# Performance work log

Hardware: AMD Instinct MI355X
Metric: run time of the kernel (lower is better)

## Reference

```python
import jax, jax.numpy as jnp
from jax import lax
import numpy as np

IN, H1, H2 = 16, 64, 1


def _init_lstm(key, in_dim, hid):
    k = 1.0 / np.sqrt(hid)
    k1, k2, k3, k4 = jax.random.split(key, 4)
    u = lambda kk, shp: jax.random.uniform(kk, shp, jnp.float32, -k, k)
    return u(k1, (4 * hid, in_dim)), u(k2, (4 * hid, hid)), u(k3, (4 * hid,)), u(k4, (4 * hid,))


def setup_inputs() -> dict:
    key = jax.random.key(0)
    kx, k1, k2, kf = jax.random.split(key, 4)
    x = jax.random.normal(kx, (4096, 256, IN), jnp.float32)
    w_ih1, w_hh1, b_ih1, b_hh1 = _init_lstm(k1, IN, H1)
    w_ih2, w_hh2, b_ih2, b_hh2 = _init_lstm(k2, H1, H2)
    kfw, kfb = jax.random.split(kf)
    fc_w = jax.random.uniform(kfw, (1, 1), jnp.float32, -1.0, 1.0)
    fc_b = jax.random.uniform(kfb, (1,), jnp.float32, -1.0, 1.0)
    return {"x": x,
            "w_ih1": w_ih1, "w_hh1": w_hh1, "b_ih1": b_ih1, "b_hh1": b_hh1,
            "w_ih2": w_ih2, "w_hh2": w_hh2, "b_ih2": b_ih2, "b_hh2": b_hh2,
            "fc_w": fc_w, "fc_b": fc_b}


def _lstm(x, w_ih, w_hh, b_ih, b_hh):
    # x: [B, T, in]; PyTorch gate order: i, f, g, o
    B = x.shape[0]
    H = w_hh.shape[1]
    # precompute input projection for all timesteps (big GEMM outside recurrence)
    xg = jnp.einsum('bti,gi->btg', x, w_ih) + b_ih + b_hh  # [B, T, 4H]

    def step(carry, xg_t):
        h, c = carry
        gates = xg_t + h @ w_hh.T  # [B, 4H]
        i, f, g, o = jnp.split(gates, 4, axis=-1)
        i = jax.nn.sigmoid(i)
        f = jax.nn.sigmoid(f)
        g = jnp.tanh(g)
        o = jax.nn.sigmoid(o)
        c = f * c + i * g
        h = o * jnp.tanh(c)
        return (h, c), h

    h0 = jnp.zeros((B, H), x.dtype)
    (_, _), hs = lax.scan(step, (h0, h0), jnp.swapaxes(xg, 0, 1))  # hs: [T, B, H]
    return jnp.swapaxes(hs, 0, 1)  # [B, T, H]


def reference(x, w_ih1, w_hh1, b_ih1, b_hh1, w_ih2, w_hh2, b_ih2, b_hh2, fc_w, fc_b):
    h = _lstm(x, w_ih1, w_hh1, b_ih1, b_hh1)   # [B, T, 64]
    h = _lstm(h, w_ih2, w_hh2, b_ih2, b_hh2)   # [B, T, 1]
    return h @ fc_w.T + fc_b                     # [B, T, 1]
```

## Files before the change

kernel.cpp:

```cpp
#include <hip/hip_runtime.h>

typedef float  f32x4  __attribute__((ext_vector_type(4)));
typedef __bf16 bf16x8 __attribute__((ext_vector_type(8)));
typedef unsigned short u16x8 __attribute__((ext_vector_type(8)));

#define NL2E (-1.44269504088896f)
#define TL2E ( 2.88539008177793f)

__device__ __forceinline__ float sigm_z(float z) {
    return __builtin_amdgcn_rcpf(1.0f + __builtin_amdgcn_exp2f(z));
}
__device__ __forceinline__ float tanh_z(float z) {
    return 1.0f - 2.0f * __builtin_amdgcn_rcpf(1.0f + __builtin_amdgcn_exp2f(z));
}

__global__ __launch_bounds__(256, 1) void lstm_fused(
    const float* __restrict__ x,
    const float* __restrict__ w_ih1,
    const float* __restrict__ w_hh1,
    const float* __restrict__ b_ih1, const float* __restrict__ b_hh1,
    const float* __restrict__ w_ih2,
    const float* __restrict__ w_hh2,
    const float* __restrict__ b_ih2, const float* __restrict__ b_hh2,
    const float* __restrict__ fc_w, const float* __restrict__ fc_b,
    float* __restrict__ out)
{
    __shared__ unsigned short A_h[2 * 16 * 64];
    __shared__ unsigned short Xc[2 * 16 * 16 * 32];
    __shared__ float Pre2[2][64];

    const int tid = threadIdx.x;
    const int wv  = tid >> 6;
    const int l   = tid & 63;
    const int q   = l & 15;
    const int hi  = l >> 4;
    const int b0  = blockIdx.x << 4;
    const int he  = (wv << 4) + q;
    const int sw  = (q & 7) << 4;

    ((u16x8*)A_h)[tid] = (u16x8){0,0,0,0,0,0,0,0};

    bf16x8 Bf[4][3];
    #pragma unroll
    for (int g = 0; g < 4; ++g) {
        const float sc = (g == 2) ? TL2E : NL2E;
        const int n = (g << 6) + (wv << 4) + q;
        #pragma unroll
        for (int ks = 0; ks < 3; ++ks) {
            bf16x8 tmp;
            #pragma unroll
            for (int j = 0; j < 8; ++j) {
                const int k = ks * 32 + hi * 8 + j;
                float v = 0.f;
                if (k < 64)      v = w_hh1[n * 64 + k];
                else if (k < 80) v = w_ih1[n * 16 + (k - 64)];
                tmp[j] = (__bf16)(sc * v);
            }
            Bf[g][ks] = tmp;
        }
    }
    bf16x8 B2[2];
    {
        const float sc2 = (q == 2) ? TL2E : NL2E;
        #pragma unroll
        for (int ks = 0; ks < 2; ++ks) {
            bf16x8 tmp;
            #pragma unroll
            for (int j = 0; j < 8; ++j) {
                const int k = ks * 32 + hi * 8 + j;
                const float v = (q < 4) ? w_ih2[q * 64 + k] : 0.f;
                tmp[j] = (__bf16)(sc2 * v);
            }
            B2[ks] = tmp;
        }
    }

    float accb[4];
    #pragma unroll
    for (int g = 0; g < 4; ++g) {
        const float sc = (g == 2) ? TL2E : NL2E;
        accb[g] = sc * (b_ih1[(g << 6) + he] + b_hh1[(g << 6) + he]);
    }

    const float w2si = NL2E * w_hh2[0], w2sf = NL2E * w_hh2[1];
    const float w2sg = TL2E * w_hh2[2], w2so = NL2E * w_hh2[3];
    const float nb2i = NL2E * (b_ih2[0] + b_hh2[0]);
    const float nb2f = NL2E * (b_ih2[1] + b_hh2[1]);
    const float tb2g = TL2E * (b_ih2[2] + b_hh2[2]);
    const float nb2o = NL2E * (b_ih2[3] + b_hh2[3]);
    const float fcw = fc_w[0], fcb = fc_b[0];

    const int bx = tid >> 4, part = tid & 15;
    const int swx = (bx & 7) << 4;
    const unsigned xo0 = (unsigned)(bx * 1024 + (((part << 6) +  0) ^ swx));
    const unsigned xo1 = (unsigned)(bx * 1024 + (((part << 6) + 16) ^ swx));
    const unsigned xo2 = (unsigned)(bx * 1024 + (((part << 6) + 32) ^ swx));
    const unsigned xo3 = (unsigned)(bx * 1024 + (((part << 6) + 48) ^ swx));
    const float* xrow = x + (size_t)(b0 + bx) * 4096 + part * 16;

    f32x4 xq0, xq1, xq2, xq3;
    auto stage_x = [&](int bufoff) {
        bf16x8 lo, hw;
        #pragma unroll
        for (int j = 0; j < 4; ++j) {
            lo[j] = (__bf16)xq0[j]; lo[4 + j] = (__bf16)xq1[j];
            hw[j] = (__bf16)xq2[j]; hw[4 + j] = (__bf16)xq3[j];
        }
        const u16x8 z = {0,0,0,0,0,0,0,0};
        char* base = (char*)Xc + bufoff;
        *(u16x8*)(base + xo0) = __builtin_bit_cast(u16x8, lo);
        *(u16x8*)(base + xo1) = __builtin_bit_cast(u16x8, hw);
        *(u16x8*)(base + xo2) = z;
        *(u16x8*)(base + xo3) = z;
    };

    xq0 = ((const f32x4*)xrow)[0]; xq1 = ((const f32x4*)xrow)[1];
    xq2 = ((const f32x4*)xrow)[2]; xq3 = ((const f32x4*)xrow)[3];
    stage_x(0);
    {
        const float* p = xrow + 256;
        xq0 = ((const f32x4*)p)[0]; xq1 = ((const f32x4*)p)[1];
        xq2 = ((const f32x4*)p)[2]; xq3 = ((const f32x4*)p)[3];
    }

    const unsigned ar0 = (unsigned)((q * 128 +      hi * 16) ^ sw);
    const unsigned ar1 = (unsigned)((q * 128 + 64 + hi * 16) ^ sw);
    unsigned awb[4];
    #pragma unroll
    for (int j = 0; j < 4; ++j) {
        const int b = (hi << 2) + j;
        awb[j] = (unsigned)(b * 128 + ((he * 2) ^ ((b & 7) << 4)));
    }

    f32x4 c1 = {0.f, 0.f, 0.f, 0.f};
    float h2 = 0.f, c2 = 0.f;

    __syncthreads();

    #pragma unroll 2
    for (int t = 0; t < 256; ++t) {
        const int tt = t & 15;
        if (tt == 0 && t + 16 < 256) {
            stage_x(((((t >> 4) + 1) & 1)) << 14);
            if (t + 32 < 256) {
                const float* p = xrow + (t + 32) * 16;
                xq0 = ((const f32x4*)p)[0]; xq1 = ((const f32x4*)p)[1];
                xq2 = ((const f32x4*)p)[2]; xq3 = ((const f32x4*)p)[3];
            }
        }

        const int rb = ((t + 1) & 1) << 11;
        const u16x8 ra0 = *(const u16x8*)((const char*)A_h + rb + ar0);
        const u16x8 ra1 = *(const u16x8*)((const char*)A_h + rb + ar1);
        const u16x8 ra2 = *(const u16x8*)((const char*)Xc + (((t >> 4) & 1) << 14)
                                          + ((q * 1024 + (tt << 6) + (hi << 4)) ^ sw));

        if (wv == 1 && t >= 2 && l < 16) {
            const f32x4 p2 = *(const f32x4*)&Pre2[(t + 1) & 1][l << 2];
            const float zi = p2[0] + __builtin_fmaf(w2si, h2, nb2i);
            const float zf = p2[1] + __builtin_fmaf(w2sf, h2, nb2f);
            const float zg = p2[2] + __builtin_fmaf(w2sg, h2, tb2g);
            const float zo = p2[3] + __builtin_fmaf(w2so, h2, nb2o);
            const float i2 = sigm_z(zi), f2v = sigm_z(zf);
            const float g2v = tanh_z(zg), o2 = sigm_z(zo);
            c2 = __builtin_fmaf(f2v, c2, i2 * g2v);
            h2 = o2 * tanh_z(c2 * TL2E);
            out[(size_t)(b0 + l) * 256 + (t - 2)] = __builtin_fmaf(fcw, h2, fcb);
        }

        const bf16x8 a0 = __builtin_bit_cast(bf16x8, ra0);
        const bf16x8 a1 = __builtin_bit_cast(bf16x8, ra1);
        const bf16x8 a2 = __builtin_bit_cast(bf16x8, ra2);

        f32x4 g0 = {accb[0], accb[0], accb[0], accb[0]};
        f32x4 g1 = {accb[1], accb[1], accb[1], accb[1]};
        f32x4 g2 = {accb[2], accb[2], accb[2], accb[2]};
        f32x4 g3 = {accb[3], accb[3], accb[3], accb[3]};
        g0 = __builtin_amdgcn_mfma_f32_16x16x32_bf16(a0, Bf[0][0], g0, 0, 0, 0);
        g1 = __builtin_amdgcn_mfma_f32_16x16x32_bf16(a0, Bf[1][0], g1, 0, 0, 0);
        g2 = __builtin_amdgcn_mfma_f32_16x16x32_bf16(a0, Bf[2][0], g2, 0, 0, 0);
        g3 = __builtin_amdgcn_mfma_f32_16x16x32_bf16(a0, Bf[3][0], g3, 0, 0, 0);
        g0 = __builtin_amdgcn_mfma_f32_16x16x32_bf16(a1, Bf[0][1], g0, 0, 0, 0);
        g1 = __builtin_amdgcn_mfma_f32_16x16x32_bf16(a1, Bf[1][1], g1, 0, 0, 0);
        g2 = __builtin_amdgcn_mfma_f32_16x16x32_bf16(a1, Bf[2][1], g2, 0, 0, 0);
        g3 = __builtin_amdgcn_mfma_f32_16x16x32_bf16(a1, Bf[3][1], g3, 0, 0, 0);
        g0 = __builtin_amdgcn_mfma_f32_16x16x32_bf16(a2, Bf[0][2], g0, 0, 0, 0);
        g1 = __builtin_amdgcn_mfma_f32_16x16x32_bf16(a2, Bf[1][2], g1, 0, 0, 0);
        g2 = __builtin_amdgcn_mfma_f32_16x16x32_bf16(a2, Bf[2][2], g2, 0, 0, 0);
        g3 = __builtin_amdgcn_mfma_f32_16x16x32_bf16(a2, Bf[3][2], g3, 0, 0, 0);

        if (wv == 3) {
            f32x4 p4 = {0.f, 0.f, 0.f, 0.f};
            p4 = __builtin_amdgcn_mfma_f32_16x16x32_bf16(a0, B2[0], p4, 0, 0, 0);
            p4 = __builtin_amdgcn_mfma_f32_16x16x32_bf16(a1, B2[1], p4, 0, 0, 0);
            if (q < 4) {
                #pragma unroll
                for (int r = 0; r < 4; ++r) Pre2[t & 1][((hi << 2) + r) * 4 + q] = p4[r];
            }
        }

        unsigned short* AW = (unsigned short*)((char*)A_h + ((t & 1) << 11));
        #pragma unroll
        for (int j = 0; j < 4; ++j) {
            const float iv = sigm_z(g0[j]);
            const float fv = sigm_z(g1[j]);
            const float gv = tanh_z(g2[j]);
            const float ov = sigm_z(g3[j]);
            const float cn = __builtin_fmaf(fv, c1[j], iv * gv);
            c1[j] = cn;
            const float hv = ov * tanh_z(cn * TL2E);
            *(unsigned short*)((char*)AW + awb[j]) = __builtin_bit_cast(unsigned short, (__bf16)hv);
        }
        __syncthreads();
    }

    if (wv == 3) {
        const u16x8 ra0 = *(const u16x8*)((const char*)A_h + 2048 + ar0);
        const u16x8 ra1 = *(const u16x8*)((const char*)A_h + 2048 + ar1);
        f32x4 p4 = {0.f, 0.f, 0.f, 0.f};
        p4 = __builtin_amdgcn_mfma_f32_16x16x32_bf16(__builtin_bit_cast(bf16x8, ra0), B2[0], p4, 0, 0, 0);
        p4 = __builtin_amdgcn_mfma_f32_16x16x32_bf16(__builtin_bit_cast(bf16x8, ra1), B2[1], p4, 0, 0, 0);
        if (q < 4) {
            #pragma unroll
            for (int r = 0; r < 4; ++r) Pre2[0][((hi << 2) + r) * 4 + q] = p4[r];
        }
    }
    if (wv == 1 && l < 16) {
        const f32x4 p2 = *(const f32x4*)&Pre2[1][l << 2];
        const float zi = p2[0] + __builtin_fmaf(w2si, h2, nb2i);
        const float zf = p2[1] + __builtin_fmaf(w2sf, h2, nb2f);
        const float zg = p2[2] + __builtin_fmaf(w2sg, h2, tb2g);
        const float zo = p2[3] + __builtin_fmaf(w2so, h2, nb2o);
        const float i2 = sigm_z(zi), f2v = sigm_z(zf);
        const float g2v = tanh_z(zg), o2 = sigm_z(zo);
        c2 = __builtin_fmaf(f2v, c2, i2 * g2v);
        h2 = o2 * tanh_z(c2 * TL2E);
        out[(size_t)(b0 + l) * 256 + 254] = __builtin_fmaf(fcw, h2, fcb);
    }
    __syncthreads();
    if (wv == 1 && l < 16) {
        const f32x4 p2 = *(const f32x4*)&Pre2[0][l << 2];
        const float zi = p2[0] + __builtin_fmaf(w2si, h2, nb2i);
        const float zf = p2[1] + __builtin_fmaf(w2sf, h2, nb2f);
        const float zg = p2[2] + __builtin_fmaf(w2sg, h2, tb2g);
        const float zo = p2[3] + __builtin_fmaf(w2so, h2, nb2o);
        const float i2 = sigm_z(zi), f2v = sigm_z(zf);
        const float g2v = tanh_z(zg), o2 = sigm_z(zo);
        c2 = __builtin_fmaf(f2v, c2, i2 * g2v);
        h2 = o2 * tanh_z(c2 * TL2E);
        out[(size_t)(b0 + l) * 256 + 255] = __builtin_fmaf(fcw, h2, fcb);
    }
}

extern "C" void kernel_launch(void* const* d_in, const int* in_sizes, int n_in,
                              void* d_out, int out_size, void* d_ws, size_t ws_size,
                              hipStream_t stream) {
    (void)in_sizes; (void)n_in; (void)out_size; (void)d_ws; (void)ws_size;
    const float* x     = (const float*)d_in[0];
    const float* w_ih1 = (const float*)d_in[1];
    const float* w_hh1 = (const float*)d_in[2];
    const float* b_ih1 = (const float*)d_in[3];
    const float* b_hh1 = (const float*)d_in[4];
    const float* w_ih2 = (const float*)d_in[5];
    const float* w_hh2 = (const float*)d_in[6];
    const float* b_ih2 = (const float*)d_in[7];
    const float* b_hh2 = (const float*)d_in[8];
    const float* fc_w  = (const float*)d_in[9];
    const float* fc_b  = (const float*)d_in[10];
    lstm_fused<<<dim3(256), dim3(256), 0, stream>>>(
        x, w_ih1, w_hh1, b_ih1, b_hh1, w_ih2, w_hh2, b_ih2, b_hh2, fc_w, fc_b,
        (float*)d_out);
}
```

Baseline: 157.0 us.

## Halve batch rows per block to 8 and launch 512 blocks at two per CU

Each block now handles 8 batch rows instead of 16 and the grid doubles to 512 blocks, with launch bounds raised to two blocks per CU so the serial 256-step recurrence is spread across more CUs. Because the 16-row MFMA tile now holds only 8 real rows, each lane evaluates the LSTM cell for two rows rather than four, which shortens the per-step activation chain. Output for layer 2 is gathered into a small shared buffer and written as 16-wide vector stores instead of one scalar store per step, and odd block groups sleep briefly at start to stagger them. The cost is half of every MFMA doing wasted work on padding rows and more register pressure at two blocks per CU.

```diff
diff --git a/kernel.cpp b/kernel.cpp
--- a/kernel.cpp
+++ b/kernel.cpp
@@ -14,7 +14,7 @@
     return 1.0f - 2.0f * __builtin_amdgcn_rcpf(1.0f + __builtin_amdgcn_exp2f(z));
 }
 
-__global__ __launch_bounds__(256, 1) void lstm_fused(
+__global__ __launch_bounds__(256, 2) void lstm_fused(
     const float* __restrict__ x,
     const float* __restrict__ w_ih1,
     const float* __restrict__ w_hh1,
@@ -25,20 +25,31 @@
     const float* __restrict__ fc_w, const float* __restrict__ fc_b,
     float* __restrict__ out)
 {
-    __shared__ unsigned short A_h[2 * 16 * 64];
-    __shared__ unsigned short Xc[2 * 16 * 16 * 32];
-    __shared__ float Pre2[2][64];
+    __shared__ unsigned short A_h[2 * 8 * 64];
+    __shared__ unsigned short Xc[2 * 8 * 16 * 32];
+    __shared__ float Pre2[2][32];
+    __shared__ float Ybuf[8][16];
 
     const int tid = threadIdx.x;
     const int wv  = tid >> 6;
     const int l   = tid & 63;
     const int q   = l & 15;
     const int hi  = l >> 4;
-    const int b0  = blockIdx.x << 4;
+    const int b0  = blockIdx.x << 3;
     const int he  = (wv << 4) + q;
-    const int sw  = (q & 7) << 4;
-
-    ((u16x8*)A_h)[tid] = (u16x8){0,0,0,0,0,0,0,0};
+
+    if ((blockIdx.x >> 8) & 1) __builtin_amdgcn_s_sleep(7);
+
+    if (tid < 128) ((u16x8*)A_h)[tid] = (u16x8){0,0,0,0,0,0,0,0};
+    {
+        const int sb = tid >> 5, sr = tid & 31, st = sr >> 1, sh = sr & 1;
+        const u16x8 z = {0,0,0,0,0,0,0,0};
+        #pragma unroll
+        for (int buf = 0; buf < 2; ++buf) {
+            *(u16x8*)((char*)Xc + buf * 8192 + sb * 1024
+                      + ((st * 64 + 32 + sh * 16) ^ (sb << 4))) = z;
+        }
+    }
 
     bf16x8 Bf[4][3];
     #pragma unroll
@@ -90,49 +101,34 @@
     const float nb2o = NL2E * (b_ih2[3] + b_hh2[3]);
     const float fcw = fc_w[0], fcb = fc_b[0];
 
-    const int bx = tid >> 4, part = tid & 15;
-    const int swx = (bx & 7) << 4;
-    const unsigned xo0 = (unsigned)(bx * 1024 + (((part << 6) +  0) ^ swx));
-    const unsigned xo1 = (unsigned)(bx * 1024 + (((part << 6) + 16) ^ swx));
-    const unsigned xo2 = (unsigned)(bx * 1024 + (((part << 6) + 32) ^ swx));
-    const unsigned xo3 = (unsigned)(bx * 1024 + (((part << 6) + 48) ^ swx));
-    const float* xrow = x + (size_t)(b0 + bx) * 4096 + part * 16;
-
-    f32x4 xq0, xq1, xq2, xq3;
+    const int sb = tid >> 5, sr = tid & 31, st = sr >> 1, sh = sr & 1;
+    const unsigned xoff = (unsigned)(sb * 1024 + ((st * 64 + sh * 16) ^ (sb << 4)));
+    const float* xrow = x + (size_t)(b0 + sb) * 4096 + st * 16 + sh * 8;
+
+    f32x4 xqa, xqb;
+    auto ldx = [&](int t) {
+        const float* p = xrow + t * 16;
+        xqa = ((const f32x4*)p)[0]; xqb = ((const f32x4*)p)[1];
+    };
     auto stage_x = [&](int bufoff) {
-        bf16x8 lo, hw;
-        #pragma unroll
-        for (int j = 0; j < 4; ++j) {
-            lo[j] = (__bf16)xq0[j]; lo[4 + j] = (__bf16)xq1[j];
-            hw[j] = (__bf16)xq2[j]; hw[4 + j] = (__bf16)xq3[j];
-        }
-        const u16x8 z = {0,0,0,0,0,0,0,0};
-        char* base = (char*)Xc + bufoff;
-        *(u16x8*)(base + xo0) = __builtin_bit_cast(u16x8, lo);
-        *(u16x8*)(base + xo1) = __builtin_bit_cast(u16x8, hw);
-        *(u16x8*)(base + xo2) = z;
-        *(u16x8*)(base + xo3) = z;
+        bf16x8 v;
+        #pragma unroll
+        for (int j = 0; j < 4; ++j) { v[j] = (__bf16)xqa[j]; v[4 + j] = (__bf16)xqb[j]; }
+        *(u16x8*)((char*)Xc + bufoff + xoff) = __builtin_bit_cast(u16x8, v);
     };
-
-    xq0 = ((const f32x4*)xrow)[0]; xq1 = ((const f32x4*)xrow)[1];
-    xq2 = ((const f32x4*)xrow)[2]; xq3 = ((const f32x4*)xrow)[3];
-    stage_x(0);
-    {
-        const float* p = xrow + 256;
-        xq0 = ((const f32x4*)p)[0]; xq1 = ((const f32x4*)p)[1];
-        xq2 = ((const f32x4*)p)[2]; xq3 = ((const f32x4*)p)[3];
-    }
-
-    const unsigned ar0 = (unsigned)((q * 128 +      hi * 16) ^ sw);
-    const unsigned ar1 = (unsigned)((q * 128 + 64 + hi * 16) ^ sw);
-    unsigned awb[4];
-    #pragma unroll
-    for (int j = 0; j < 4; ++j) {
-        const int b = (hi << 2) + j;
-        awb[j] = (unsigned)(b * 128 + ((he * 2) ^ ((b & 7) << 4)));
-    }
-
-    f32x4 c1 = {0.f, 0.f, 0.f, 0.f};
+    ldx(0); stage_x(0); ldx(16);
+
+    const int rb = q & 7;
+    const unsigned ar0 = (unsigned)(rb * 128 + ((hi * 16)      ^ (rb << 4)));
+    const unsigned ar1 = (unsigned)(rb * 128 + ((64 + hi * 16) ^ (rb << 4)));
+    const unsigned xro = (unsigned)(rb * 1024);
+    const unsigned xrs = (unsigned)(hi * 16);
+    const int bA = ((hi & 1) << 2) + ((hi >> 1) << 1);
+    const int bB = bA + 1;
+    const unsigned awA = (unsigned)(bA * 128 + ((he * 2) ^ (bA << 4)));
+    const unsigned awB = (unsigned)(bB * 128 + ((he * 2) ^ (bB << 4)));
+
+    float cA = 0.f, cB = 0.f;
     float h2 = 0.f, c2 = 0.f;
 
     __syncthreads();
@@ -141,21 +137,17 @@
     for (int t = 0; t < 256; ++t) {
         const int tt = t & 15;
         if (tt == 0 && t + 16 < 256) {
-            stage_x(((((t >> 4) + 1) & 1)) << 14);
-            if (t + 32 < 256) {
-                const float* p = xrow + (t + 32) * 16;
-                xq0 = ((const f32x4*)p)[0]; xq1 = ((const f32x4*)p)[1];
-                xq2 = ((const f32x4*)p)[2]; xq3 = ((const f32x4*)p)[3];
-            }
-        }
-
-        const int rb = ((t + 1) & 1) << 11;
-        const u16x8 ra0 = *(const u16x8*)((const char*)A_h + rb + ar0);
-        const u16x8 ra1 = *(const u16x8*)((const char*)A_h + rb + ar1);
-        const u16x8 ra2 = *(const u16x8*)((const char*)Xc + (((t >> 4) & 1) << 14)
-                                          + ((q * 1024 + (tt << 6) + (hi << 4)) ^ sw));
-
-        if (wv == 1 && t >= 2 && l < 16) {
+            stage_x((((t >> 4) + 1) & 1) << 13);
+            if (t + 32 < 256) ldx(t + 32);
+        }
+
+        const int rbo = ((t + 1) & 1) << 10;
+        const u16x8 ra0 = *(const u16x8*)((const char*)A_h + rbo + ar0);
+        const u16x8 ra1 = *(const u16x8*)((const char*)A_h + rbo + ar1);
+        const u16x8 ra2 = *(const u16x8*)((const char*)Xc + (((t >> 4) & 1) << 13)
+                                          + xro + (((tt << 6) + xrs) ^ (rb << 4)));
+
+        if (wv == 1 && l < 8 && t >= 2) {
             const f32x4 p2 = *(const f32x4*)&Pre2[(t + 1) & 1][l << 2];
             const float zi = p2[0] + __builtin_fmaf(w2si, h2, nb2i);
             const float zf = p2[1] + __builtin_fmaf(w2sf, h2, nb2f);
@@ -165,7 +157,14 @@
             const float g2v = tanh_z(zg), o2 = sigm_z(zo);
             c2 = __builtin_fmaf(f2v, c2, i2 * g2v);
             h2 = o2 * tanh_z(c2 * TL2E);
-            out[(size_t)(b0 + l) * 256 + (t - 2)] = __builtin_fmaf(fcw, h2, fcb);
+            const int s = t - 2;
+            Ybuf[l][s & 15] = __builtin_fmaf(fcw, h2, fcb);
+            if ((s & 15) == 15) {
+                float* op = out + (size_t)(b0 + l) * 256 + (s - 15);
+                const f32x4* yb = (const f32x4*)Ybuf[l];
+                ((f32x4*)op)[0] = yb[0]; ((f32x4*)op)[1] = yb[1];
+                ((f32x4*)op)[2] = yb[2]; ((f32x4*)op)[3] = yb[3];
+            }
         }
 
         const bf16x8 a0 = __builtin_bit_cast(bf16x8, ra0);
@@ -193,62 +192,66 @@
             f32x4 p4 = {0.f, 0.f, 0.f, 0.f};
             p4 = __builtin_amdgcn_mfma_f32_16x16x32_bf16(a0, B2[0], p4, 0, 0, 0);
             p4 = __builtin_amdgcn_mfma_f32_16x16x32_bf16(a1, B2[1], p4, 0, 0, 0);
-            if (q < 4) {
+            if (hi < 2 && q < 4) {
                 #pragma unroll
-                for (int r = 0; r < 4; ++r) Pre2[t & 1][((hi << 2) + r) * 4 + q] = p4[r];
-            }
-        }
-
-        unsigned short* AW = (unsigned short*)((char*)A_h + ((t & 1) << 11));
-        #pragma unroll
-        for (int j = 0; j < 4; ++j) {
-            const float iv = sigm_z(g0[j]);
-            const float fv = sigm_z(g1[j]);
-            const float gv = tanh_z(g2[j]);
-            const float ov = sigm_z(g3[j]);
-            const float cn = __builtin_fmaf(fv, c1[j], iv * gv);
-            c1[j] = cn;
-            const float hv = ov * tanh_z(cn * TL2E);
-            *(unsigned short*)((char*)AW + awb[j]) = __builtin_bit_cast(unsigned short, (__bf16)hv);
+                for (int r = 0; r < 4; ++r) Pre2[t & 1][(((hi << 2) + r) << 2) + q] = p4[r];
+            }
+        }
+
+        const bool lo = (hi < 2);
+        const float zIA = lo ? g0[0] : g0[2], zIB = lo ? g0[1] : g0[3];
+        const float zFA = lo ? g1[0] : g1[2], zFB = lo ? g1[1] : g1[3];
+        const float zGA = lo ? g2[0] : g2[2], zGB = lo ? g2[1] : g2[3];
+        const float zOA = lo ? g3[0] : g3[2], zOB = lo ? g3[1] : g3[3];
+
+        char* AW = (char*)A_h + ((t & 1) << 10);
+        {
+            const float iv = sigm_z(zIA), fv = sigm_z(zFA);
+            const float gv = tanh_z(zGA), ov = sigm_z(zOA);
+            cA = __builtin_fmaf(fv, cA, iv * gv);
+            const float hv = ov * tanh_z(cA * TL2E);
+            *(unsigned short*)(AW + awA) = __builtin_bit_cast(unsigned short, (__bf16)hv);
+        }
+        {
+            const float iv = sigm_z(zIB), fv = sigm_z(zFB);
+            const float gv = tanh_z(zGB), ov = sigm_z(zOB);
+            cB = __builtin_fmaf(fv, cB, iv * gv);
+            const float hv = ov * tanh_z(cB * TL2E);
+            *(unsigned short*)(AW + awB) = __builtin_bit_cast(unsigned short, (__bf16)hv);
         }
         __syncthreads();
     }
 
     if (wv == 3) {
-        const u16x8 ra0 = *(const u16x8*)((const char*)A_h + 2048 + ar0);
-        const u16x8 ra1 = *(const u16x8*)((const char*)A_h + 2048 + ar1);
+        const u16x8 ra0 = *(const u16x8*)((const char*)A_h + 1024 + ar0);
+        const u16x8 ra1 = *(const u16x8*)((const char*)A_h + 1024 + ar1);
         f32x4 p4 = {0.f, 0.f, 0.f, 0.f};
         p4 = __builtin_amdgcn_mfma_f32_16x16x32_bf16(__builtin_bit_cast(bf16x8, ra0), B2[0], p4, 0, 0, 0);
         p4 = __builtin_amdgcn_mfma_f32_16x16x32_bf16(__builtin_bit_cast(bf16x8, ra1), B2[1], p4, 0, 0, 0);
-        if (q < 4) {
+        if (hi < 2 && q < 4) {
             #pragma unroll
-            for (int r = 0; r < 4; ++r) Pre2[0][((hi << 2) + r) * 4 + q] = p4[r];
-        }
-    }
-    if (wv == 1 && l < 16) {
-        const f32x4 p2 = *(const f32x4*)&Pre2[1][l << 2];
-        const float zi = p2[0] + __builtin_fmaf(w2si, h2, nb2i);
-        const float zf = p2[1] + __builtin_fmaf(w2sf, h2, nb2f);
-        const float zg = p2[2] + __builtin_fmaf(w2sg, h2, tb2g);
-        const float zo = p2[3] + __builtin_fmaf(w2so, h2, nb2o);
-        const float i2 = sigm_z(zi), f2v = sigm_z(zf);
-        const float g2v = tanh_z(zg), o2 = sigm_z(zo);
-        c2 = __builtin_fmaf(f2v, c2, i2 * g2v);
-        h2 = o2 * tanh_z(c2 * TL2E);
-        out[(size_t)(b0 + l) * 256 + 254] = __builtin_fmaf(fcw, h2, fcb);
+            for (int r = 0; r < 4; ++r) Pre2[0][(((hi << 2) + r) << 2) + q] = p4[r];
+        }
     }
     __syncthreads();
-    if (wv == 1 && l < 16) {
-        const f32x4 p2 = *(const f32x4*)&Pre2[0][l << 2];
-        const float zi = p2[0] + __builtin_fmaf(w2si, h2, nb2i);
-        const float zf = p2[1] + __builtin_fmaf(w2sf, h2, nb2f);
-        const float zg = p2[2] + __builtin_fmaf(w2sg, h2, tb2g);
-        const float zo = p2[3] + __builtin_fmaf(w2so, h2, nb2o);
-        const float i2 = sigm_z(zi), f2v = sigm_z(zf);
-        const float g2v = tanh_z(zg), o2 = sigm_z(zo);
-        c2 = __builtin_fmaf(f2v, c2, i2 * g2v);
-        h2 = o2 * tanh_z(c2 * TL2E);
-        out[(size_t)(b0 + l) * 256 + 255] = __builtin_fmaf(fcw, h2, fcb);
+    if (wv == 1 && l < 8) {
+        #pragma unroll
+        for (int e = 0; e < 2; ++e) {
+            const f32x4 p2 = *(const f32x4*)&Pre2[1 - e][l << 2];
+            const float zi = p2[0] + __builtin_fmaf(w2si, h2, nb2i);
+            const float zf = p2[1] + __builtin_fmaf(w2sf, h2, nb2f);
+            const float zg = p2[2] + __builtin_fmaf(w2sg, h2, tb2g);
+            const float zo = p2[3] + __builtin_fmaf(w2so, h2, nb2o);
+            const float i2 = sigm_z(zi), f2v = sigm_z(zf);
+            const float g2v = tanh_z(zg), o2 = sigm_z(zo);
+            c2 = __builtin_fmaf(f2v, c2, i2 * g2v);
+            h2 = o2 * tanh_z(c2 * TL2E);
+            Ybuf[l][14 + e] = __builtin_fmaf(fcw, h2, fcb);
+        }
+        float* op = out + (size_t)(b0 + l) * 256 + 240;
+        const f32x4* yb = (const f32x4*)Ybuf[l];
+        ((f32x4*)op)[0] = yb[0]; ((f32x4*)op)[1] = yb[1];
+        ((f32x4*)op)[2] = yb[2]; ((f32x4*)op)[3] = yb[3];
     }
 }
 
@@ -267,7 +270,7 @@
     const float* b_hh2 = (const float*)d_in[8];
     const float* fc_w  = (const float*)d_in[9];
     const float* fc_b  = (const float*)d_in[10];
-    lstm_fused<<<dim3(256), dim3(256), 0, stream>>>(
+    lstm_fused<<<dim3(512), dim3(256), 0, stream>>>(
         x, w_ih1, w_hh1, b_ih1, b_hh1, w_ih2, w_hh2, b_ih2, b_hh2, fc_w, fc_b,
         (float*)d_out);
 }
```

Measured after the change: 161.8 us. 3.0% more time.

## Fuse LSTM gate activations algebraically, batch layer-2 outputs, use raw barrier

Applied to the files above, without the earlier changes.

Replaces the separate sigmoid and tanh calls with a fused cell update that combines the input and cell gates into one reciprocal, and the output gate and cell tanh into another. This cuts the rcp count per element from five to three, and the cell pre-activation is clamped to avoid overflow. Layer-2 outputs are staged in a small shared buffer and written as 16-byte vector stores every 16 steps instead of scattered scalar stores. The per-step __syncthreads is replaced by an inline s_waitcnt lgkmcnt(0) plus s_barrier, which may skip waiting on outstanding global memory operations.

```diff
diff --git a/kernel.cpp b/kernel.cpp
--- a/kernel.cpp
+++ b/kernel.cpp
@@ -7,11 +7,17 @@
 #define NL2E (-1.44269504088896f)
 #define TL2E ( 2.88539008177793f)
 
-__device__ __forceinline__ float sigm_z(float z) {
-    return __builtin_amdgcn_rcpf(1.0f + __builtin_amdgcn_exp2f(z));
-}
-__device__ __forceinline__ float tanh_z(float z) {
-    return 1.0f - 2.0f * __builtin_amdgcn_rcpf(1.0f + __builtin_amdgcn_exp2f(z));
+__device__ __forceinline__ float cell_update(float zi, float zf, float zg, float zo, float& c) {
+    const float Ei = __builtin_amdgcn_exp2f(zi);
+    const float Ef = __builtin_amdgcn_exp2f(zf);
+    const float Eg = __builtin_amdgcn_exp2f(zg);
+    const float Eo = __builtin_amdgcn_exp2f(zo);
+    const float ig = (Eg - 1.0f) * __builtin_amdgcn_rcpf((1.0f + Ei) * (1.0f + Eg));
+    const float fv = __builtin_amdgcn_rcpf(1.0f + Ef);
+    c = __builtin_fmaf(fv, c, ig);
+    const float zc = fminf(fmaxf(TL2E * c, -60.0f), 60.0f);
+    const float Ec = __builtin_amdgcn_exp2f(zc);
+    return (Ec - 1.0f) * __builtin_amdgcn_rcpf((1.0f + Eo) * (1.0f + Ec));
 }
 
 __global__ __launch_bounds__(256, 1) void lstm_fused(
@@ -28,6 +34,7 @@
     __shared__ unsigned short A_h[2 * 16 * 64];
     __shared__ unsigned short Xc[2 * 16 * 16 * 32];
     __shared__ float Pre2[2][64];
+    __shared__ float Ybuf[16][16];
 
     const int tid = threadIdx.x;
     const int wv  = tid >> 6;
@@ -132,7 +139,7 @@
         awb[j] = (unsigned)(b * 128 + ((he * 2) ^ ((b & 7) << 4)));
     }
 
-    f32x4 c1 = {0.f, 0.f, 0.f, 0.f};
+    float c1[4] = {0.f, 0.f, 0.f, 0.f};
     float h2 = 0.f, c2 = 0.f;
 
     __syncthreads();
@@ -155,17 +162,21 @@
         const u16x8 ra2 = *(const u16x8*)((const char*)Xc + (((t >> 4) & 1) << 14)
                                           + ((q * 1024 + (tt << 6) + (hi << 4)) ^ sw));
 
-        if (wv == 1 && t >= 2 && l < 16) {
-            const f32x4 p2 = *(const f32x4*)&Pre2[(t + 1) & 1][l << 2];
-            const float zi = p2[0] + __builtin_fmaf(w2si, h2, nb2i);
-            const float zf = p2[1] + __builtin_fmaf(w2sf, h2, nb2f);
-            const float zg = p2[2] + __builtin_fmaf(w2sg, h2, tb2g);
-            const float zo = p2[3] + __builtin_fmaf(w2so, h2, nb2o);
-            const float i2 = sigm_z(zi), f2v = sigm_z(zf);
-            const float g2v = tanh_z(zg), o2 = sigm_z(zo);
-            c2 = __builtin_fmaf(f2v, c2, i2 * g2v);
-            h2 = o2 * tanh_z(c2 * TL2E);
-            out[(size_t)(b0 + l) * 256 + (t - 2)] = __builtin_fmaf(fcw, h2, fcb);
+        if (wv == 1 && t >= 2) {
+            const int s = t - 2;
+            if (l < 16) {
+                const f32x4 p2 = *(const f32x4*)&Pre2[(t + 1) & 1][l << 2];
+                const float zi = p2[0] + __builtin_fmaf(w2si, h2, nb2i);
+                const float zf = p2[1] + __builtin_fmaf(w2sf, h2, nb2f);
+                const float zg = p2[2] + __builtin_fmaf(w2sg, h2, tb2g);
+                const float zo = p2[3] + __builtin_fmaf(w2so, h2, nb2o);
+                h2 = cell_update(zi, zf, zg, zo, c2);
+                Ybuf[l][s & 15] = __builtin_fmaf(fcw, h2, fcb);
+            }
+            if ((s & 15) == 15) {
+                float* op = out + (size_t)(b0 + (l >> 2)) * 256 + (s - 15) + ((l & 3) << 2);
+                *(f32x4*)op = *(const f32x4*)&Ybuf[l >> 2][(l & 3) << 2];
+            }
         }
 
         const bf16x8 a0 = __builtin_bit_cast(bf16x8, ra0);
@@ -199,19 +210,14 @@
             }
         }
 
-        unsigned short* AW = (unsigned short*)((char*)A_h + ((t & 1) << 11));
+        char* AW = (char*)A_h + ((t & 1) << 11);
         #pragma unroll
         for (int j = 0; j < 4; ++j) {
-            const float iv = sigm_z(g0[j]);
-            const float fv = sigm_z(g1[j]);
-            const float gv = tanh_z(g2[j]);
-            const float ov = sigm_z(g3[j]);
-            const float cn = __builtin_fmaf(fv, c1[j], iv * gv);
-            c1[j] = cn;
-            const float hv = ov * tanh_z(cn * TL2E);
-            *(unsigned short*)((char*)AW + awb[j]) = __builtin_bit_cast(unsigned short, (__bf16)hv);
-        }
-        __syncthreads();
+            const float hv = cell_update(g0[j], g1[j], g2[j], g3[j], c1[j]);
+            *(unsigned short*)(AW + awb[j]) = __builtin_bit_cast(unsigned short, (__bf16)hv);
+        }
+
+        asm volatile("s_waitcnt lgkmcnt(0)\n\ts_barrier" ::: "memory");
     }
 
     if (wv == 3) {
@@ -225,30 +231,22 @@
             for (int r = 0; r < 4; ++r) Pre2[0][((hi << 2) + r) * 4 + q] = p4[r];
         }
     }
-    if (wv == 1 && l < 16) {
-        const f32x4 p2 = *(const f32x4*)&Pre2[1][l << 2];
-        const float zi = p2[0] + __builtin_fmaf(w2si, h2, nb2i);
-        const float zf = p2[1] + __builtin_fmaf(w2sf, h2, nb2f);
-        const float zg = p2[2] + __builtin_fmaf(w2sg, h2, tb2g);
-        const float zo = p2[3] + __builtin_fmaf(w2so, h2, nb2o);
-        const float i2 = sigm_z(zi), f2v = sigm_z(zf);
-        const float g2v = tanh_z(zg), o2 = sigm_z(zo);
-        c2 = __builtin_fmaf(f2v, c2, i2 * g2v);
-        h2 = o2 * tanh_z(c2 * TL2E);
-        out[(size_t)(b0 + l) * 256 + 254] = __builtin_fmaf(fcw, h2, fcb);
-    }
     __syncthreads();
-    if (wv == 1 && l < 16) {
-        const f32x4 p2 = *(const f32x4*)&Pre2[0][l << 2];
-        const float zi = p2[0] + __builtin_fmaf(w2si, h2, nb2i);
-        const float zf = p2[1] + __builtin_fmaf(w2sf, h2, nb2f);
-        const float zg = p2[2] + __builtin_fmaf(w2sg, h2, tb2g);
-        const float zo = p2[3] + __builtin_fmaf(w2so, h2, nb2o);
-        const float i2 = sigm_z(zi), f2v = sigm_z(zf);
-        const float g2v = tanh_z(zg), o2 = sigm_z(zo);
-        c2 = __builtin_fmaf(f2v, c2, i2 * g2v);
-        h2 = o2 * tanh_z(c2 * TL2E);
-        out[(size_t)(b0 + l) * 256 + 255] = __builtin_fmaf(fcw, h2, fcb);
+    if (wv == 1) {
+        if (l < 16) {
+            #pragma unroll
+            for (int e = 0; e < 2; ++e) {
+                const f32x4 p2 = *(const f32x4*)&Pre2[1 - e][l << 2];
+                const float zi = p2[0] + __builtin_fmaf(w2si, h2, nb2i);
+                const float zf = p2[1] + __builtin_fmaf(w2sf, h2, nb2f);
+                const float zg = p2[2] + __builtin_fmaf(w2sg, h2, tb2g);
+                const float zo = p2[3] + __builtin_fmaf(w2so, h2, nb2o);
+                h2 = cell_update(zi, zf, zg, zo, c2);
+                Ybuf[l][14 + e] = __builtin_fmaf(fcw, h2, fcb);
+            }
+        }
+        float* op = out + (size_t)(b0 + (l >> 2)) * 256 + 240 + ((l & 3) << 2);
+        *(f32x4*)op = *(const f32x4*)&Ybuf[l >> 2][(l & 3) << 2];
     }
 }
 
```

New measurement: 160.3 us. +2.1%, slower.
